# Kernel tuning notes

Measured on AMD Instinct MI355X. Metric: run time of the kernel, lower is better.

## Reference

```python
import jax, jax.numpy as jnp
import numpy as np
import math

B, S, D, H = 4, 1024, 4096, 32
HD = D // H  # 128


def _rope(t, cos, sin):
    # t: [B,S,H,HD]; cos/sin: [S, HD//2]
    tr = t.reshape(*t.shape[:-1], HD // 2, 2)
    re, im = tr[..., 0], tr[..., 1]
    c = cos[None, :, None, :]
    s = sin[None, :, None, :]
    out_re = re * c - im * s
    out_im = re * s + im * c
    return jnp.stack([out_re, out_im], axis=-1).reshape(t.shape)


def setup_inputs() -> dict:
    key = jax.random.key(0)
    ks = jax.random.split(key, 6)
    wscale = 1.0 / math.sqrt(D)
    x = jax.random.normal(ks[0], (B, S, D), dtype=jnp.float32)
    wq = jax.random.normal(ks[1], (D, D), dtype=jnp.float32) * wscale
    wk = jax.random.normal(ks[2], (D, D), dtype=jnp.float32) * wscale
    wv = jax.random.normal(ks[3], (D, D), dtype=jnp.float32) * wscale
    wo = jax.random.normal(ks[4], (D, D), dtype=jnp.float32) * wscale
    # standard LLaMA RoPE frequencies: theta = 10000^{-2i/HD}
    inv_freq = 1.0 / (10000.0 ** (np.arange(0, HD, 2, dtype=np.float32) / HD))
    angles = np.arange(S, dtype=np.float32)[:, None] * inv_freq[None, :]  # [S, HD//2]
    freqs_cos = jnp.asarray(np.cos(angles), dtype=jnp.float32)
    freqs_sin = jnp.asarray(np.sin(angles), dtype=jnp.float32)
    # causal mask, additive, 0 on/below diagonal, -inf above
    mask = jnp.where(jnp.tril(jnp.ones((S, S), dtype=bool)), 0.0, -jnp.inf)
    mask = mask[None, None].astype(jnp.float32)  # [1,1,S,S]
    return {"x": x, "wq": wq, "wk": wk, "wv": wv, "wo": wo,
            "freqs_cos": freqs_cos, "freqs_sin": freqs_sin, "mask": mask}


def reference(x, wq, wk, wv, wo, freqs_cos, freqs_sin, mask):
    # projections (torch Linear: y = x @ W^T)
    xq = (x @ wq.T).reshape(B, S, H, HD)
    xk = (x @ wk.T).reshape(B, S, H, HD)
    xv = (x @ wv.T).reshape(B, S, H, HD)
    xq = _rope(xq, freqs_cos, freqs_sin)
    xk = _rope(xk, freqs_cos, freqs_sin)
    # prefill (start_pos == 0): keys/values are xk/xv
    scores = jnp.einsum('bshd,bthd->bhst', xq, xk) / math.sqrt(HD)
    scores = scores + mask
    probs = jax.nn.softmax(scores.astype(jnp.float32), axis=-1).astype(xq.dtype)
    out = jnp.einsum('bhst,bthd->bshd', probs, xv).reshape(B, S, D)
    return out @ wo.T
```

## Files before the change

### kernel.cpp

```cpp
#include <hip/hip_runtime.h>
#include <hip/hip_bf16.h>


typedef __bf16 bf16_t;
typedef bf16_t bf16x8 __attribute__((ext_vector_type(8)));
typedef bf16_t bf16x4 __attribute__((ext_vector_type(4)));
typedef bf16_t bf16x2 __attribute__((ext_vector_type(2)));
typedef float  f32x4  __attribute__((ext_vector_type(4)));

#define DDIM 4096
#define NTILES 64
#define NEG_INF (-__builtin_inff())
#define MFMA16(a,b,c) __builtin_amdgcn_mfma_f32_16x16x32_bf16(a,b,c,0,0,0)

__device__ __forceinline__ void gl_lds16(const bf16_t* g, bf16_t* l) {
    __builtin_amdgcn_global_load_lds((__attribute__((address_space(1))) void*)(g),
                                     (__attribute__((address_space(3))) void*)(l), 16, 0, 0);
}

__global__ __launch_bounds__(256)
void cvt_k(const float* __restrict__ src, bf16_t* __restrict__ dst, int n8)
{
    const int stride = gridDim.x * 256;
    for (int i = blockIdx.x * 256 + threadIdx.x; i < n8; i += stride) {
        const float* s = src + (size_t)i * 8;
        f32x4 a = *(const f32x4*)(s);
        f32x4 b = *(const f32x4*)(s + 4);
        bf16x8 o;
        o[0] = (bf16_t)a.x; o[1] = (bf16_t)a.y; o[2] = (bf16_t)a.z; o[3] = (bf16_t)a.w;
        o[4] = (bf16_t)b.x; o[5] = (bf16_t)b.y; o[6] = (bf16_t)b.z; o[7] = (bf16_t)b.w;
        *(bf16x8*)(dst + (size_t)i * 8) = o;
    }
}


__device__ __forceinline__ void stage_half(const bf16_t* __restrict__ A,
    const bf16_t* __restrict__ Bm, int m0, int n0, int kt, int hh,
    bf16_t* __restrict__ sb, int wave, int lane)
{
#pragma unroll
    for (int j = 0; j < 2; ++j) {
        const int chunk = wave * 2 + j;
        int row0;
        if (hh == 0)      row0 = chunk * 8;
        else if (hh == 1) row0 = 128 + chunk * 8;
        else if (hh == 2) row0 = (chunk < 8) ? chunk * 8 : 64 + chunk * 8;
        else              row0 = (chunk < 8) ? 64 + chunk * 8 : 128 + chunk * 8;
        const bool isB = (hh < 2);
        const int grow = (isB ? n0 : m0) + row0 + (lane >> 3);
        const int gcol = kt + (((lane & 7) ^ (lane >> 3)) << 3);
        const bf16_t* gp = (isB ? Bm : A) + (size_t)grow * DDIM + gcol;
        gl_lds16(gp, sb + (isB ? 16384 : 0) + row0 * 64);
    }
}

template<int STG>
__device__ __forceinline__ void ktile(const bf16_t* __restrict__ A,
    const bf16_t* __restrict__ Bm, int m0, int n0, int t,
    bf16_t* __restrict__ sb, bf16_t* __restrict__ sbn,
    int wave, int lane, int quad, int r, int wm, int wn,
    f32x4 acc[4][2][4], bf16x8 bfrag[4][2])
{
    const int kx0 = (quad ^ (r & 7)) << 3;
    const int kx1 = ((4 + quad) ^ (r & 7)) << 3;
    {
        bf16x8 af[2][2];
#pragma unroll
        for (int nf = 0; nf < 4; ++nf) {
            const int ro = 16384 + (((wn << 6) + (nf << 4) + r) << 6);
            bfrag[nf][0] = *(const bf16x8*)(sb + ro + kx0);
            bfrag[nf][1] = *(const bf16x8*)(sb + ro + kx1);
        }
#pragma unroll
        for (int mf = 0; mf < 2; ++mf) {
            const int ro = ((wm << 7) + (mf << 4) + r) << 6;
            af[mf][0] = *(const bf16x8*)(sb + ro + kx0);
            af[mf][1] = *(const bf16x8*)(sb + ro + kx1);
        }
        if (STG >= 1) stage_half(A, Bm, m0, n0, (t + 1) << 6, 3, sbn, wave, lane);
        __builtin_amdgcn_sched_barrier(0);
        __builtin_amdgcn_s_barrier();
        asm volatile("s_waitcnt lgkmcnt(0)" ::: "memory");
        __builtin_amdgcn_sched_barrier(0);
        __builtin_amdgcn_s_setprio(1);
#pragma unroll
        for (int kk = 0; kk < 2; ++kk)
#pragma unroll
            for (int mf = 0; mf < 2; ++mf)
#pragma unroll
                for (int nf = 0; nf < 4; ++nf)
                    acc[0][mf][nf] = MFMA16(af[mf][kk], bfrag[nf][kk], acc[0][mf][nf]);
        __builtin_amdgcn_s_setprio(0);
        __builtin_amdgcn_sched_barrier(0);
        __builtin_amdgcn_s_barrier();
    }
#pragma unroll
    for (int q = 1; q < 4; ++q) {
        bf16x8 af[2][2];
#pragma unroll
        for (int mf = 0; mf < 2; ++mf) {
            const int ro = ((wm << 7) + (q << 5) + (mf << 4) + r) << 6;
            af[mf][0] = *(const bf16x8*)(sb + ro + kx0);
            af[mf][1] = *(const bf16x8*)(sb + ro + kx1);
        }
        if (STG == 2) stage_half(A, Bm, m0, n0, (t + 2) << 6, q - 1, sb, wave, lane);
        __builtin_amdgcn_sched_barrier(0);
        __builtin_amdgcn_s_barrier();
        asm volatile("s_waitcnt lgkmcnt(0)" ::: "memory");
        __builtin_amdgcn_sched_barrier(0);
        __builtin_amdgcn_s_setprio(1);
#pragma unroll
        for (int kk = 0; kk < 2; ++kk)
#pragma unroll
            for (int mf = 0; mf < 2; ++mf)
#pragma unroll
                for (int nf = 0; nf < 4; ++nf)
                    acc[q][mf][nf] = MFMA16(af[mf][kk], bfrag[nf][kk], acc[q][mf][nf]);
        __builtin_amdgcn_s_setprio(0);
        if (q == 3) {
            if (STG == 2)      asm volatile("s_waitcnt vmcnt(6)" ::: "memory");
            else if (STG == 1) asm volatile("s_waitcnt vmcnt(0)" ::: "memory");
        }
        __builtin_amdgcn_sched_barrier(0);
        __builtin_amdgcn_s_barrier();
    }
}

template<bool C_F32>
__global__ __launch_bounds__(512, 2)
void gemm256(const bf16_t* __restrict__ A, const bf16_t* __restrict__ Bm, void* __restrict__ Cv)
{
    __shared__ __attribute__((aligned(16))) bf16_t sm[2 * 32768];
    const int tid  = threadIdx.x;
    const int wave = tid >> 6, lane = tid & 63;
    const int quad = lane >> 4, r = lane & 15;
    const int wm = wave >> 2, wn = wave & 3;
    const int swz = ((int)blockIdx.x % 8) * 32 + (int)blockIdx.x / 8;
    const int m0 = (swz >> 4) << 8, n0 = (swz & 15) << 8;

    f32x4 acc[4][2][4] = {};
    bf16x8 bfrag[4][2];

#pragma unroll
    for (int hh = 0; hh < 4; ++hh) stage_half(A, Bm, m0, n0, 0, hh, sm, wave, lane);
#pragma unroll
    for (int hh = 0; hh < 3; ++hh) stage_half(A, Bm, m0, n0, 64, hh, sm + 32768, wave, lane);
    asm volatile("s_waitcnt vmcnt(6)" ::: "memory");
    __builtin_amdgcn_s_barrier();

#pragma unroll 2
    for (int t = 0; t < NTILES - 2; ++t) {
        bf16_t* sb  = sm + ((t & 1) ? 32768 : 0);
        bf16_t* sbn = sm + ((t & 1) ? 0 : 32768);
        ktile<2>(A, Bm, m0, n0, t, sb, sbn, wave, lane, quad, r, wm, wn, acc, bfrag);
    }
    ktile<1>(A, Bm, m0, n0, NTILES - 2, sm, sm + 32768, wave, lane, quad, r, wm, wn, acc, bfrag);
    ktile<0>(A, Bm, m0, n0, NTILES - 1, sm + 32768, sm, wave, lane, quad, r, wm, wn, acc, bfrag);

#pragma unroll
    for (int q = 0; q < 4; ++q)
#pragma unroll
        for (int mf = 0; mf < 2; ++mf)
#pragma unroll
            for (int reg = 0; reg < 4; ++reg) {
                const size_t row = (size_t)(m0 + (wm << 7) + (q << 5) + (mf << 4)
                                            + (quad << 2) + reg) * DDIM;
#pragma unroll
                for (int nf = 0; nf < 4; ++nf) {
                    const size_t idx = row + n0 + (wn << 6) + (nf << 4) + r;
                    if constexpr (C_F32) ((float*)Cv)[idx] = acc[q][mf][nf][reg];
                    else                 ((bf16_t*)Cv)[idx] = (bf16_t)acc[q][mf][nf][reg];
                }
            }
}

__global__ void rope_k(bf16_t* __restrict__ q, bf16_t* __restrict__ k,
                       const float* __restrict__ fc, const float* __restrict__ fs)
{
    const int p   = blockIdx.x * 256 + threadIdx.x;
    const int bs  = p >> 11;
    const int rem = p & 2047;
    const int s   = bs & 1023;
    const int h   = rem >> 6;
    const int pp  = rem & 63;
    const size_t off = (size_t)bs * DDIM + h * 128 + pp * 2;
    const float c  = fc[s * 64 + pp];
    const float sn = fs[s * 64 + pp];
    bf16x2 qv = *(bf16x2*)(q + off);
    bf16x2 kv = *(bf16x2*)(k + off);
    const float qre = (float)qv.x, qim = (float)qv.y;
    const float kre = (float)kv.x, kim = (float)kv.y;
    bf16x2 qo, ko;
    qo.x = (bf16_t)(qre * c - qim * sn);
    qo.y = (bf16_t)(qre * sn + qim * c);
    ko.x = (bf16_t)(kre * c - kim * sn);
    ko.y = (bf16_t)(kre * sn + kim * c);
    *(bf16x2*)(q + off) = qo;
    *(bf16x2*)(k + off) = ko;
}

__global__ __launch_bounds__(256, 2)
void attn_k(const bf16_t* __restrict__ qm, const bf16_t* __restrict__ km,
            const bf16_t* __restrict__ vm, bf16_t* __restrict__ om)
{
    constexpr int BQ = 128, BT = 64;
    constexpr int PS = 80;
    __shared__ __attribute__((aligned(16))) bf16_t sK[BT * 128];
    __shared__ __attribute__((aligned(16))) bf16_t sVt[128 * 64];
    __shared__ __attribute__((aligned(16))) bf16_t sP[4][32 * PS];
    const int tid = threadIdx.x, wave = tid >> 6, lane = tid & 63;
    const int quad = lane >> 4, r = lane & 15;
    const int b = blockIdx.x >> 5, h = blockIdx.x & 31;
    const int q0 = (7 - (int)blockIdx.y) * BQ;
    const int qw = q0 + wave * 32;
    const float scale = 0.08838834764831845f;

    bf16x8 qf[2][4];
#pragma unroll
    for (int mt = 0; mt < 2; ++mt)
#pragma unroll
        for (int kk = 0; kk < 4; ++kk)
            qf[mt][kk] = *(const bf16x8*)(qm + (size_t)(b * 1024 + qw + mt * 16 + r) * DDIM
                                          + h * 128 + kk * 32 + quad * 8);

    f32x4 oacc[2][8] = {};
    float m_i[2][4], l_i[2][4];
#pragma unroll
    for (int mt = 0; mt < 2; ++mt)
#pragma unroll
        for (int reg = 0; reg < 4; ++reg) { m_i[mt][reg] = NEG_INF; l_i[mt][reg] = 0.f; }

    const bf16_t* gKb = km + (size_t)(b * 1024 + wave * 16 + quad) * DDIM + h * 128;
    const int rp = tid >> 3, cseg = tid & 7;

    for (int t0 = 0; t0 < q0 + BQ; t0 += BT) {
#pragma unroll
        for (int i = 0; i < 4; ++i) {
            const int xv = (i * 4 + quad) & 7;
            gl_lds16(gKb + (size_t)(t0 + i * 4) * DDIM + ((r ^ xv) << 3),
                     sK + (wave * 4 + i) * 512);
        }
        {
            const bf16_t* gv = vm + (size_t)(b * 1024 + t0 + 2 * rp) * DDIM + h * 128 + cseg * 16;
            bf16x8 v00 = *(const bf16x8*)(gv);
            bf16x8 v01 = *(const bf16x8*)(gv + 8);
            bf16x8 v10 = *(const bf16x8*)(gv + DDIM);
            bf16x8 v11 = *(const bf16x8*)(gv + DDIM + 8);
#pragma unroll
            for (int e = 0; e < 8; ++e) {
                bf16x2 w0, w1;
                w0.x = v00[e]; w0.y = v10[e];
                w1.x = v01[e]; w1.y = v11[e];
                const int pb = ((((rp >> 2) ^ (e ^ cseg)) & 7) << 3) + ((rp & 3) << 1);
                *(bf16x2*)(sVt + (cseg * 16 + e) * 64 + pb) = w0;
                *(bf16x2*)(sVt + (cseg * 16 + 8 + e) * 64 + pb) = w1;
            }
        }
        __syncthreads();

        f32x4 sacc[2][4] = {};
#pragma unroll
        for (int kk = 0; kk < 4; ++kk) {
            bf16x8 kf[4];
#pragma unroll
            for (int nt = 0; nt < 4; ++nt)
                kf[nt] = *(const bf16x8*)(sK + (nt * 16 + r) * 128
                                          + (((kk * 4 + quad) ^ (r & 7)) << 3));
#pragma unroll
            for (int mt = 0; mt < 2; ++mt)
#pragma unroll
                for (int nt = 0; nt < 4; ++nt)
                    sacc[mt][nt] = MFMA16(qf[mt][kk], kf[nt], sacc[mt][nt]);
        }

#pragma unroll
        for (int mt = 0; mt < 2; ++mt) {
#pragma unroll
            for (int reg = 0; reg < 4; ++reg) {
                const int qrow = qw + mt * 16 + quad * 4 + reg;
                float mx = NEG_INF;
#pragma unroll
                for (int nt = 0; nt < 4; ++nt) {
                    const int tcol = t0 + nt * 16 + r;
                    float v = sacc[mt][nt][reg] * scale;
                    v = (tcol <= qrow) ? v : NEG_INF;
                    sacc[mt][nt][reg] = v;
                    mx = fmaxf(mx, v);
                }
                mx = fmaxf(mx, __shfl_xor(mx, 1));
                mx = fmaxf(mx, __shfl_xor(mx, 2));
                mx = fmaxf(mx, __shfl_xor(mx, 4));
                mx = fmaxf(mx, __shfl_xor(mx, 8));
                if (!__all(mx - m_i[mt][reg] <= 8.0f)) {
                    const float mnew = fmaxf(m_i[mt][reg], mx);
                    const float alpha = __expf(m_i[mt][reg] - mnew);
                    m_i[mt][reg] = mnew;
                    l_i[mt][reg] *= alpha;
#pragma unroll
                    for (int nt = 0; nt < 8; ++nt)
                        oacc[mt][nt][reg] *= alpha;
                }
                float rs = 0.f;
#pragma unroll
                for (int nt = 0; nt < 4; ++nt) {
                    const float pv = __expf(sacc[mt][nt][reg] - m_i[mt][reg]);
                    rs += pv;
                    sP[wave][(mt * 16 + quad * 4 + reg) * PS + nt * 16 + r] = (bf16_t)pv;
                }
                rs += __shfl_xor(rs, 1);
                rs += __shfl_xor(rs, 2);
                rs += __shfl_xor(rs, 4);
                rs += __shfl_xor(rs, 8);
                l_i[mt][reg] += rs;
            }
        }

#pragma unroll
        for (int kk2 = 0; kk2 < 2; ++kk2) {
            bf16x8 pf[2];
#pragma unroll
            for (int mt = 0; mt < 2; ++mt)
                pf[mt] = *(const bf16x8*)(&sP[wave][(mt * 16 + r) * PS + kk2 * 32 + quad * 8]);
#pragma unroll
            for (int nt = 0; nt < 8; ++nt) {
                bf16x8 vf = *(const bf16x8*)(sVt + (nt * 16 + r) * 64
                                             + ((((kk2 * 4 + quad) ^ (r & 7) ^ nt) & 7) << 3));
#pragma unroll
                for (int mt = 0; mt < 2; ++mt)
                    oacc[mt][nt] = MFMA16(pf[mt], vf, oacc[mt][nt]);
            }
        }
        __syncthreads();
    }

#pragma unroll
    for (int mt = 0; mt < 2; ++mt)
#pragma unroll
        for (int reg = 0; reg < 4; ++reg) {
            const float inv = 1.0f / l_i[mt][reg];
            const size_t row = (size_t)(b * 1024 + qw + mt * 16 + quad * 4 + reg) * DDIM + h * 128;
#pragma unroll
            for (int nt = 0; nt < 8; ++nt)
                om[row + nt * 16 + r] = (bf16_t)(oacc[mt][nt][reg] * inv);
        }
}

extern "C" void kernel_launch(void* const* d_in, const int* in_sizes, int n_in,
                              void* d_out, int out_size, void* d_ws, size_t ws_size,
                              hipStream_t stream)
{
    (void)in_sizes; (void)n_in; (void)out_size; (void)d_ws; (void)ws_size;
    const float* x  = (const float*)d_in[0];
    const float* wq = (const float*)d_in[1];
    const float* wk = (const float*)d_in[2];
    const float* wv = (const float*)d_in[3];
    const float* wo = (const float*)d_in[4];
    const float* fc = (const float*)d_in[5];
    const float* fs = (const float*)d_in[6];

    const size_t NE = (size_t)DDIM * DDIM;
    const int n8 = (int)(NE / 8);

    bf16_t* wkb = (bf16_t*)d_out;
    bf16_t* wvb = wkb + NE;
    bf16_t* xb  = (bf16_t*)d_in[2];
    bf16_t* wqb = xb + NE;
    bf16_t* wob = (bf16_t*)d_in[3];
    bf16_t* ob  = wob + NE;
    bf16_t* kb  = (bf16_t*)d_in[1];
    bf16_t* vb  = kb + NE;
    bf16_t* qb  = (bf16_t*)d_in[4];
    float*  out = (float*)d_out;

    cvt_k<<<2048, 256, 0, stream>>>(wk, wkb, n8);
    cvt_k<<<2048, 256, 0, stream>>>(wv, wvb, n8);
    cvt_k<<<2048, 256, 0, stream>>>(x,  xb,  n8);
    cvt_k<<<2048, 256, 0, stream>>>(wq, wqb, n8);
    cvt_k<<<2048, 256, 0, stream>>>(wo, wob, n8);

    gemm256<false><<<256, 512, 0, stream>>>(xb, wkb, kb);
    gemm256<false><<<256, 512, 0, stream>>>(xb, wvb, vb);
    gemm256<false><<<256, 512, 0, stream>>>(xb, wqb, qb);
    rope_k<<<32768, 256, 0, stream>>>(qb, kb, fc, fs);
    attn_k<<<dim3(128, 8), 256, 0, stream>>>(qb, kb, vb, ob);
    gemm256<true><<<256, 512, 0, stream>>>(ob, wob, out);
}
```

Baseline: 851.9 us.

## Fuse QKV GEMMs into one launch with RoPE epilogue and batch conversions

Merges the three projection GEMMs into a single grid-z launch and applies RoPE in the GEMM epilogue using lane shuffles, which removes the separate rope kernel and its extra read/write pass over Q and K. The five fp32→bf16 conversion launches are collapsed into two multi-tensor launches. A partial lgkmcnt wait is also inserted before the barrier in the first k sub-step. The combined launch puts 768 blocks in flight at once, which may improve tail utilisation but changes cache behaviour, and the epilogue now performs scattered loads of the cos/sin tables.

Measured after the change: 884.6 us. +3.8%, slower.

```diff
diff --git a/kernel.cpp b/kernel.cpp
--- a/kernel.cpp
+++ b/kernel.cpp
@@ -19,8 +19,14 @@
 }
 
 __global__ __launch_bounds__(256)
-void cvt_k(const float* __restrict__ src, bf16_t* __restrict__ dst, int n8)
-{
+void cvt3_k(const float* __restrict__ s0, bf16_t* __restrict__ d0,
+            const float* __restrict__ s1, bf16_t* __restrict__ d1,
+            const float* __restrict__ s2, bf16_t* __restrict__ d2, int n8)
+{
+    const float* src; bf16_t* dst;
+    if (blockIdx.y == 0)      { src = s0; dst = d0; }
+    else if (blockIdx.y == 1) { src = s1; dst = d1; }
+    else                      { src = s2; dst = d2; }
     const int stride = gridDim.x * 256;
     for (int i = blockIdx.x * 256 + threadIdx.x; i < n8; i += stride) {
         const float* s = src + (size_t)i * 8;
@@ -78,6 +84,7 @@
             af[mf][1] = *(const bf16x8*)(sb + ro + kx1);
         }
         if (STG >= 1) stage_half(A, Bm, m0, n0, (t + 1) << 6, 3, sbn, wave, lane);
+        asm volatile("s_waitcnt lgkmcnt(8)" ::: "memory");
         __builtin_amdgcn_sched_barrier(0);
         __builtin_amdgcn_s_barrier();
         asm volatile("s_waitcnt lgkmcnt(0)" ::: "memory");
@@ -127,8 +134,9 @@
 }
 
 template<bool C_F32>
-__global__ __launch_bounds__(512, 2)
-void gemm256(const bf16_t* __restrict__ A, const bf16_t* __restrict__ Bm, void* __restrict__ Cv)
+__device__ __forceinline__ void gemm_body(const bf16_t* __restrict__ A,
+    const bf16_t* __restrict__ Bm, void* __restrict__ Cv,
+    const float* __restrict__ fc, const float* __restrict__ fs, bool doRope)
 {
     __shared__ __attribute__((aligned(16))) bf16_t sm[2 * 32768];
     const int tid  = threadIdx.x;
@@ -157,46 +165,51 @@
     ktile<1>(A, Bm, m0, n0, NTILES - 2, sm, sm + 32768, wave, lane, quad, r, wm, wn, acc, bfrag);
     ktile<0>(A, Bm, m0, n0, NTILES - 1, sm + 32768, sm, wave, lane, quad, r, wm, wn, acc, bfrag);
 
+    const float sgn = (r & 1) ? 1.0f : -1.0f;
 #pragma unroll
     for (int q = 0; q < 4; ++q)
 #pragma unroll
         for (int mf = 0; mf < 2; ++mf)
 #pragma unroll
             for (int reg = 0; reg < 4; ++reg) {
-                const size_t row = (size_t)(m0 + (wm << 7) + (q << 5) + (mf << 4)
-                                            + (quad << 2) + reg) * DDIM;
+                const int grow = m0 + (wm << 7) + (q << 5) + (mf << 4) + (quad << 2) + reg;
+                const size_t rowoff = (size_t)grow * DDIM;
+                const int s = grow & 1023;
 #pragma unroll
                 for (int nf = 0; nf < 4; ++nf) {
-                    const size_t idx = row + n0 + (wn << 6) + (nf << 4) + r;
-                    if constexpr (C_F32) ((float*)Cv)[idx] = acc[q][mf][nf][reg];
-                    else                 ((bf16_t*)Cv)[idx] = (bf16_t)acc[q][mf][nf][reg];
+                    float v = acc[q][mf][nf][reg];
+                    if (doRope) {
+                        const int p = ((wn & 1) << 5) + (nf << 3) + (r >> 1);
+                        const float c  = fc[s * 64 + p];
+                        const float sn = fs[s * 64 + p];
+                        const float partner = __shfl_xor(v, 1);
+                        v = v * c + sgn * partner * sn;
+                    }
+                    const size_t idx = rowoff + n0 + (wn << 6) + (nf << 4) + r;
+                    if constexpr (C_F32) ((float*)Cv)[idx] = v;
+                    else                 ((bf16_t*)Cv)[idx] = (bf16_t)v;
                 }
             }
 }
 
-__global__ void rope_k(bf16_t* __restrict__ q, bf16_t* __restrict__ k,
-                       const float* __restrict__ fc, const float* __restrict__ fs)
-{
-    const int p   = blockIdx.x * 256 + threadIdx.x;
-    const int bs  = p >> 11;
-    const int rem = p & 2047;
-    const int s   = bs & 1023;
-    const int h   = rem >> 6;
-    const int pp  = rem & 63;
-    const size_t off = (size_t)bs * DDIM + h * 128 + pp * 2;
-    const float c  = fc[s * 64 + pp];
-    const float sn = fs[s * 64 + pp];
-    bf16x2 qv = *(bf16x2*)(q + off);
-    bf16x2 kv = *(bf16x2*)(k + off);
-    const float qre = (float)qv.x, qim = (float)qv.y;
-    const float kre = (float)kv.x, kim = (float)kv.y;
-    bf16x2 qo, ko;
-    qo.x = (bf16_t)(qre * c - qim * sn);
-    qo.y = (bf16_t)(qre * sn + qim * c);
-    ko.x = (bf16_t)(kre * c - kim * sn);
-    ko.y = (bf16_t)(kre * sn + kim * c);
-    *(bf16x2*)(q + off) = qo;
-    *(bf16x2*)(k + off) = ko;
+__global__ __launch_bounds__(512, 2)
+void gemm_qkv(const bf16_t* __restrict__ A,
+              const bf16_t* __restrict__ b0, const bf16_t* __restrict__ b1,
+              const bf16_t* __restrict__ b2,
+              bf16_t* __restrict__ c0, bf16_t* __restrict__ c1, bf16_t* __restrict__ c2,
+              const float* __restrict__ fc, const float* __restrict__ fs)
+{
+    const int sel = blockIdx.z;
+    const bf16_t* Bm = (sel == 0) ? b0 : (sel == 1) ? b1 : b2;
+    bf16_t*       Cv = (sel == 0) ? c0 : (sel == 1) ? c1 : c2;
+    gemm_body<false>(A, Bm, Cv, fc, fs, sel != 1);
+}
+
+__global__ __launch_bounds__(512, 2)
+void gemm_out(const bf16_t* __restrict__ A, const bf16_t* __restrict__ Bm,
+              float* __restrict__ Cv)
+{
+    gemm_body<true>(A, Bm, Cv, nullptr, nullptr, false);
 }
 
 __global__ __launch_bounds__(256, 2)
@@ -372,16 +385,10 @@
     bf16_t* qb  = (bf16_t*)d_in[4];
     float*  out = (float*)d_out;
 
-    cvt_k<<<2048, 256, 0, stream>>>(wk, wkb, n8);
-    cvt_k<<<2048, 256, 0, stream>>>(wv, wvb, n8);
-    cvt_k<<<2048, 256, 0, stream>>>(x,  xb,  n8);
-    cvt_k<<<2048, 256, 0, stream>>>(wq, wqb, n8);
-    cvt_k<<<2048, 256, 0, stream>>>(wo, wob, n8);
-
-    gemm256<false><<<256, 512, 0, stream>>>(xb, wkb, kb);
-    gemm256<false><<<256, 512, 0, stream>>>(xb, wvb, vb);
-    gemm256<false><<<256, 512, 0, stream>>>(xb, wqb, qb);
-    rope_k<<<32768, 256, 0, stream>>>(qb, kb, fc, fs);
+    cvt3_k<<<dim3(2048, 2), 256, 0, stream>>>(wk, wkb, wv, wvb, wv, wvb, n8);
+    cvt3_k<<<dim3(2048, 3), 256, 0, stream>>>(x, xb, wq, wqb, wo, wob, n8);
+
+    gemm_qkv<<<dim3(256, 1, 3), 512, 0, stream>>>(xb, wkb, wvb, wqb, kb, vb, qb, fc, fs);
     attn_k<<<dim3(128, 8), 256, 0, stream>>>(qb, kb, vb, ob);
-    gemm256<true><<<256, 512, 0, stream>>>(ob, wob, out);
-}
+    gemm_out<<<256, 512, 0, stream>>>(ob, wob, out);
+}
```
